# Performance work log

Measured on AMD Instinct MI355X. Metric: run time of the kernel, lower is better.

Reference implementation:

```python
import jax, jax.numpy as jnp
import numpy as np

N = 100000      # nodes
E = 1600000     # edges
IN = 64         # in_feats
H = 64          # h_feats
L = 4           # num_conv_layers
FC = 2          # num_fc_layers
G = 512         # num graphs in batch
EPS = 1e-5      # BatchNorm eps


def _bn(x, g, b):
    # training-mode BatchNorm1d: batch stats (biased variance), affine
    m = x.mean(axis=0)
    v = x.var(axis=0)
    return (x - m) * jax.lax.rsqrt(v + EPS) * g + b


def setup_inputs() -> dict:
    key = jax.random.key(0)
    ks = jax.random.split(key, 12)
    x = jax.random.normal(ks[0], (N, IN), jnp.float32)
    edge_index = jax.random.randint(ks[1], (2, E), 0, N)
    batch = jnp.sort(jax.random.randint(ks[2], (N,), 0, G))
    s_in = 1.0 / np.sqrt(IN)
    s_h = 1.0 / np.sqrt(H)
    return {
        "x": x,
        "edge_index": edge_index,
        "batch": batch,
        "bn_feat_g": jnp.ones((IN,), jnp.float32),
        "bn_feat_b": jnp.zeros((IN,), jnp.float32),
        "lin_feat_W": jax.random.normal(ks[3], (IN, H), jnp.float32) * s_in,
        "lin_feat_b": jnp.zeros((H,), jnp.float32),
        "bn_conv_g": jnp.ones((L, H), jnp.float32),
        "bn_conv_b": jnp.zeros((L, H), jnp.float32),
        "conv_W": jax.random.normal(ks[4], (L, H, H), jnp.float32) * s_h,
        "conv_b": jnp.zeros((L, H), jnp.float32),
        "bn_fc_g": jnp.ones((FC, H), jnp.float32),
        "bn_fc_b": jnp.zeros((FC, H), jnp.float32),
        "fc_W": jax.random.normal(ks[5], (FC, H, H), jnp.float32) * s_h,
        "fc_b": jnp.zeros((FC, H), jnp.float32),
        "bn_hid_g": jnp.ones((H,), jnp.float32),
        "bn_hid_b": jnp.zeros((H,), jnp.float32),
    }


def reference(x, edge_index, batch, bn_feat_g, bn_feat_b, lin_feat_W, lin_feat_b,
              bn_conv_g, bn_conv_b, conv_W, conv_b, bn_fc_g, bn_fc_b, fc_W, fc_b,
              bn_hid_g, bn_hid_b):
    # --- GCN symmetric normalization with self-loops (computed once) ---
    loop = jnp.arange(N)
    src = jnp.concatenate([edge_index[0], loop])   # source j
    dst = jnp.concatenate([edge_index[1], loop])   # target i
    deg = jax.ops.segment_sum(jnp.ones((E + N,), x.dtype), dst, num_segments=N)
    dinv = jnp.where(deg > 0, 1.0, 0.0) / jnp.sqrt(jnp.where(deg > 0, deg, 1.0))
    norm = dinv[src] * dinv[dst]                   # [E+N]

    # --- stem ---
    h = _bn(x, bn_feat_g, bn_feat_b)
    h = jax.nn.relu(h @ lin_feat_W + lin_feat_b)

    # --- stacked GCNConv + BN + ReLU + residual ---
    for i in range(L):
        h_ = _bn(h, bn_conv_g[i], bn_conv_b[i])
        m = h_ @ conv_W[i]                                    # [N,H]
        agg = jax.ops.segment_sum(norm[:, None] * m[src], dst, num_segments=N)
        h = h + jax.nn.relu(agg + conv_b[i])                  # residual=True

    # --- global add pool over graphs ---
    h = jax.ops.segment_sum(h, batch, num_segments=G)         # [G,H]

    # --- fc head ---
    for i in range(FC):
        h_ = _bn(h, bn_fc_g[i], bn_fc_b[i])
        h = jax.nn.relu(h_ @ fc_W[i] + fc_b[i])

    return _bn(h, bn_hid_g, bn_hid_b)
```

## Files before the change

kernel.cpp:

```cpp
#include <hip/hip_runtime.h>
#include <hip/hip_bf16.h>

#define NN 100000
#define EE 1600000
#define GG 512
#define NB ((NN + 255) / 256)

__global__ void deg_kernel(const int* __restrict__ ei, int* __restrict__ cnt, int E_) {
    int e = blockIdx.x * 256 + threadIdx.x;
    if (e < E_) atomicAdd(&cnt[ei[E_ + e]], 1);
}

__global__ void dinv_kernel(const int* __restrict__ cnt, float* __restrict__ dinv, int n) {
    int i = blockIdx.x * 256 + threadIdx.x;
    if (i < n) dinv[i] = rsqrtf((float)cnt[i] + 1.0f);
}

__global__ void blocksum(const int* __restrict__ cnt, int* __restrict__ bsum) {
    __shared__ int sh[256];
    int i = blockIdx.x * 256 + threadIdx.x;
    sh[threadIdx.x] = (i < NN) ? cnt[i] : 0;
    __syncthreads();
    for (int o = 128; o > 0; o >>= 1) {
        if (threadIdx.x < o) sh[threadIdx.x] += sh[threadIdx.x + o];
        __syncthreads();
    }
    if (threadIdx.x == 0) bsum[blockIdx.x] = sh[0];
}

__global__ void scan_bsum(int* __restrict__ bsum, int nb) {
    __shared__ int sh[512];
    int t = threadIdx.x;
    int v = (t < nb) ? bsum[t] : 0;
    int orig = v;
    sh[t] = v;
    __syncthreads();
    for (int o = 1; o < 512; o <<= 1) {
        int add = (t >= o) ? sh[t - o] : 0;
        __syncthreads();
        sh[t] += add;
        __syncthreads();
    }
    if (t < nb) bsum[t] = sh[t] - orig;
}

__global__ void scan_final(const int* __restrict__ cnt, const int* __restrict__ boff,
                           int* __restrict__ row_ptr, int* __restrict__ cursor) {
    __shared__ int sh[256];
    int i = blockIdx.x * 256 + threadIdx.x;
    int v = (i < NN) ? cnt[i] : 0;
    int orig = v;
    sh[threadIdx.x] = v;
    __syncthreads();
    for (int o = 1; o < 256; o <<= 1) {
        int add = (threadIdx.x >= o) ? sh[threadIdx.x - o] : 0;
        __syncthreads();
        sh[threadIdx.x] += add;
        __syncthreads();
    }
    if (i < NN) {
        int ex = boff[blockIdx.x] + sh[threadIdx.x] - orig;
        row_ptr[i] = ex;
        cursor[i] = ex;
    }
    if (i == 0) row_ptr[NN] = EE;
}

__global__ void fill_csr(const int* __restrict__ ei, const float* __restrict__ dinv,
                         int* __restrict__ cursor, int* __restrict__ csr_src,
                         float* __restrict__ csr_norm, int E_) {
    int e = blockIdx.x * 256 + threadIdx.x;
    if (e < E_) {
        int s = ei[e], d = ei[E_ + e];
        int pos = atomicAdd(&cursor[d], 1);
        csr_src[pos] = s;
        csr_norm[pos] = dinv[s] * dinv[d];
    }
}

__global__ void colstats(const float* __restrict__ A, int nrows, float* __restrict__ stats) {
    __shared__ float ssum[4][64];
    __shared__ float ssq[4][64];
    int tid = threadIdx.x;
    int col = tid & 63, rg = tid >> 6;
    float s = 0.f, q = 0.f;
    for (int r = blockIdx.x * 4 + rg; r < nrows; r += gridDim.x * 4) {
        float v = A[r * 64 + col];
        s += v;
        q = fmaf(v, v, q);
    }
    ssum[rg][col] = s; ssq[rg][col] = q;
    __syncthreads();
    if (tid < 64) {
        float ts = ssum[0][tid] + ssum[1][tid] + ssum[2][tid] + ssum[3][tid];
        float tq = ssq[0][tid] + ssq[1][tid] + ssq[2][tid] + ssq[3][tid];
        atomicAdd(&stats[tid], ts);
        atomicAdd(&stats[64 + tid], tq);
    }
}

__global__ void prep(const float* __restrict__ stats, float count,
                     const float* __restrict__ g, const float* __restrict__ b,
                     const float* __restrict__ W, const float* __restrict__ basebias,
                     float* __restrict__ Wp, float* __restrict__ bp) {
    int j = threadIdx.x;
    float acc = basebias ? basebias[j] : 0.f;
    for (int k = 0; k < 64; k++) {
        float mu  = stats[k] / count;
        float var = fmaxf(stats[64 + k] / count - mu * mu, 0.f);
        float rstd = rsqrtf(var + 1e-5f);
        float a = rstd * g[k];
        float w = W[k * 64 + j];
        Wp[k * 64 + j] = a * w;
        acc = fmaf(b[k] - mu * a, w, acc);
    }
    bp[j] = acc;
}

__global__ __launch_bounds__(256) void gemm64(const float* __restrict__ A,
                                              const float* __restrict__ Wp,
                                              const float* __restrict__ bp,
                                              float* __restrict__ C, int nrows, int dorelu,
                                              float* __restrict__ stats) {
    __shared__ float Ws[64 * 64];
    __shared__ float As[64 * 64];
    __shared__ float ssh[256];
    __shared__ float qsh[256];
    int tid = threadIdx.x;
    int row0 = blockIdx.x * 64;
    for (int i = tid; i < 4096; i += 256) {
        Ws[i] = Wp[i];
        int r = row0 + (i >> 6);
        As[i] = (r < nrows) ? A[row0 * 64 + i] : 0.f;
    }
    __syncthreads();
    int col = tid & 63;
    int rg = tid >> 6;
    float bcol = bp[col];
    float s = 0.f, q = 0.f;
    for (int rr = rg; rr < 64; rr += 4) {
        int r = row0 + rr;
        if (r >= nrows) break;
        float acc = bcol;
#pragma unroll
        for (int k = 0; k < 64; k++) acc = fmaf(As[rr * 64 + k], Ws[k * 64 + col], acc);
        float v = dorelu ? fmaxf(acc, 0.f) : acc;
        C[r * 64 + col] = v;
        s += v;
        q = fmaf(v, v, q);
    }
    if (stats) {
        ssh[tid] = s; qsh[tid] = q;
        __syncthreads();
        if (tid < 64) {
            float ts = ssh[tid] + ssh[64 + tid] + ssh[128 + tid] + ssh[192 + tid];
            float tq = qsh[tid] + qsh[64 + tid] + qsh[128 + tid] + qsh[192 + tid];
            atomicAdd(&stats[tid], ts);
            atomicAdd(&stats[64 + tid], tq);
        }
    }
}

__global__ __launch_bounds__(256) void gather(const int* __restrict__ row_ptr,
                                              const int* __restrict__ csr_src,
                                              const float* __restrict__ csr_norm,
                                              const float* __restrict__ dinv,
                                              const float* __restrict__ m,
                                              float* __restrict__ h,
                                              const float* __restrict__ cb,
                                              float* __restrict__ stats,
                                              float* __restrict__ pooled,
                                              const int* __restrict__ batch,
                                              int writeH) {
    int tid = threadIdx.x;
    int ng = tid >> 4;
    int cl = tid & 15;
    const float4* cb4 = (const float4*)cb;
    float4 cbv = cb4[cl];
    float sx = 0.f, sy = 0.f, sz = 0.f, sw = 0.f;
    float qx = 0.f, qy = 0.f, qz = 0.f, qw = 0.f;
    for (int i = blockIdx.x * 16 + ng; i < NN; i += gridDim.x * 16) {
        float di = dinv[i];
        float4 mi = ((const float4*)(m + i * 64))[cl];
        float d2 = di * di;
        float ax = d2 * mi.x, ay = d2 * mi.y, az = d2 * mi.z, aw = d2 * mi.w;
        int e0 = row_ptr[i], e1 = row_ptr[i + 1];
        for (int e = e0; e < e1; e++) {
            int s = csr_src[e];
            float w = csr_norm[e];
            float4 ms = ((const float4*)(m + s * 64))[cl];
            ax = fmaf(w, ms.x, ax);
            ay = fmaf(w, ms.y, ay);
            az = fmaf(w, ms.z, az);
            aw = fmaf(w, ms.w, aw);
        }
        float4 hb = ((const float4*)(h + i * 64))[cl];
        float nx = hb.x + fmaxf(ax + cbv.x, 0.f);
        float ny = hb.y + fmaxf(ay + cbv.y, 0.f);
        float nz = hb.z + fmaxf(az + cbv.z, 0.f);
        float nw = hb.w + fmaxf(aw + cbv.w, 0.f);
        if (writeH) {
            float4 o; o.x = nx; o.y = ny; o.z = nz; o.w = nw;
            ((float4*)(h + i * 64))[cl] = o;
        }
        if (stats) {
            sx += nx; sy += ny; sz += nz; sw += nw;
            qx = fmaf(nx, nx, qx); qy = fmaf(ny, ny, qy);
            qz = fmaf(nz, nz, qz); qw = fmaf(nw, nw, qw);
        }
        if (pooled) {
            int g = batch[i];
            float* p = pooled + g * 64 + cl * 4;
            atomicAdd(p + 0, nx);
            atomicAdd(p + 1, ny);
            atomicAdd(p + 2, nz);
            atomicAdd(p + 3, nw);
        }
    }
    if (stats) {
        __shared__ float rs[256 * 4];
        __shared__ float rq[256 * 4];
        rs[tid * 4 + 0] = sx; rs[tid * 4 + 1] = sy; rs[tid * 4 + 2] = sz; rs[tid * 4 + 3] = sw;
        rq[tid * 4 + 0] = qx; rq[tid * 4 + 1] = qy; rq[tid * 4 + 2] = qz; rq[tid * 4 + 3] = qw;
        __syncthreads();
        if (tid < 64) {
            int cl2 = tid >> 2, k = tid & 3;
            float a = 0.f, b = 0.f;
            for (int g = 0; g < 16; g++) {
                a += rs[(g * 16 + cl2) * 4 + k];
                b += rq[(g * 16 + cl2) * 4 + k];
            }
            atomicAdd(&stats[tid], a);
            atomicAdd(&stats[64 + tid], b);
        }
    }
}

__global__ void bn_apply(const float* __restrict__ A, const float* __restrict__ stats, float count,
                         const float* __restrict__ g, const float* __restrict__ b,
                         float* __restrict__ out, int total) {
    int idx = blockIdx.x * 256 + threadIdx.x;
    if (idx < total) {
        int j = idx & 63;
        float mu  = stats[j] / count;
        float var = fmaxf(stats[64 + j] / count - mu * mu, 0.f);
        float rstd = rsqrtf(var + 1e-5f);
        out[idx] = (A[idx] - mu) * rstd * g[j] + b[j];
    }
}

extern "C" void kernel_launch(void* const* d_in, const int* in_sizes, int n_in,
                              void* d_out, int out_size, void* d_ws, size_t ws_size,
                              hipStream_t stream) {
    const float* x     = (const float*)d_in[0];
    const int*   ei    = (const int*)d_in[1];
    const int*   batch = (const int*)d_in[2];
    const float* bnfg  = (const float*)d_in[3];
    const float* bnfb  = (const float*)d_in[4];
    const float* linW  = (const float*)d_in[5];
    const float* linb  = (const float*)d_in[6];
    const float* bncg  = (const float*)d_in[7];
    const float* bncb  = (const float*)d_in[8];
    const float* convW = (const float*)d_in[9];
    const float* convb = (const float*)d_in[10];
    const float* bnfcg = (const float*)d_in[11];
    const float* bnfcb = (const float*)d_in[12];
    const float* fcW   = (const float*)d_in[13];
    const float* fcb   = (const float*)d_in[14];
    const float* bnhg  = (const float*)d_in[15];
    const float* bnhb  = (const float*)d_in[16];

    const int N64 = NN * 64;
    float* ws = (float*)d_ws;
    size_t o = 0;
    int*   cnt      = (int*)(ws + o);   o += 100352;
    float* dinv     = ws + o;           o += 100352;
    int*   row_ptr  = (int*)(ws + o);   o += 100352;
    int*   cursor   = (int*)(ws + o);   o += 100352;
    int*   bsum     = (int*)(ws + o);   o += 512;
    int*   csr_src  = (int*)(ws + o);   o += EE;
    float* csr_norm = ws + o;           o += EE;
    float* h        = ws + o;           o += N64;
    float* m        = ws + o;           o += N64;
    float* statsA   = ws + o;           o += 128;
    float* statsB   = ws + o;           o += 128;
    float* Wp       = ws + o;           o += 4096;
    float* bp       = ws + o;           o += 64;
    float* pa       = ws + o;           o += GG * 64;
    float* pb       = ws + o;           o += GG * 64;

    hipMemsetAsync(cnt, 0, NN * sizeof(int), stream);
    deg_kernel<<<(EE + 255) / 256, 256, 0, stream>>>(ei, cnt, EE);
    dinv_kernel<<<NB, 256, 0, stream>>>(cnt, dinv, NN);
    blocksum<<<NB, 256, 0, stream>>>(cnt, bsum);
    scan_bsum<<<1, 512, 0, stream>>>(bsum, NB);
    scan_final<<<NB, 256, 0, stream>>>(cnt, bsum, row_ptr, cursor);
    fill_csr<<<(EE + 255) / 256, 256, 0, stream>>>(ei, dinv, cursor, csr_src, csr_norm, EE);

    hipMemsetAsync(statsA, 0, 512, stream);
    colstats<<<256, 256, 0, stream>>>(x, NN, statsA);
    prep<<<1, 64, 0, stream>>>(statsA, (float)NN, bnfg, bnfb, linW, linb, Wp, bp);
    hipMemsetAsync(statsB, 0, 512, stream);
    gemm64<<<(NN + 63) / 64, 256, 0, stream>>>(x, Wp, bp, h, NN, 1, statsB);

    hipMemsetAsync(pa, 0, GG * 64 * sizeof(float), stream);
    float* cur = statsB; float* nxt = statsA;
    for (int l = 0; l < 4; l++) {
        prep<<<1, 64, 0, stream>>>(cur, (float)NN, bncg + 64 * l, bncb + 64 * l,
                                   convW + 4096 * l, nullptr, Wp, bp);
        gemm64<<<(NN + 63) / 64, 256, 0, stream>>>(h, Wp, bp, m, NN, 0, nullptr);
        if (l < 3) {
            hipMemsetAsync(nxt, 0, 512, stream);
            gather<<<1024, 256, 0, stream>>>(row_ptr, csr_src, csr_norm, dinv, m, h,
                                             convb + 64 * l, nxt, nullptr, batch, 1);
        } else {
            gather<<<1024, 256, 0, stream>>>(row_ptr, csr_src, csr_norm, dinv, m, h,
                                             convb + 64 * l, nullptr, pa, batch, 0);
        }
        float* t = cur; cur = nxt; nxt = t;
    }

    float* pin = pa; float* pout = pb;
    for (int i = 0; i < 2; i++) {
        hipMemsetAsync(statsA, 0, 512, stream);
        colstats<<<8, 256, 0, stream>>>(pin, GG, statsA);
        prep<<<1, 64, 0, stream>>>(statsA, (float)GG, bnfcg + 64 * i, bnfcb + 64 * i,
                                   fcW + 4096 * i, fcb + 64 * i, Wp, bp);
        gemm64<<<(GG + 63) / 64, 256, 0, stream>>>(pin, Wp, bp, pout, GG, 1, nullptr);
        float* t = pin; pin = pout; pout = t;
    }

    hipMemsetAsync(statsA, 0, 512, stream);
    colstats<<<8, 256, 0, stream>>>(pin, GG, statsA);
    bn_apply<<<(GG * 64 + 255) / 256, 256, 0, stream>>>(pin, statsA, (float)GG, bnhg, bnhb,
                                                        (float*)d_out, GG * 64);
}
```

Baseline: 1.290 ms.

## Interleave CSR src/norm, unroll gather edge loop, one node per thread group

```diff
diff --git a/kernel.cpp b/kernel.cpp
--- a/kernel.cpp
+++ b/kernel.cpp
@@ -67,14 +67,15 @@
 }
 
 __global__ void fill_csr(const int* __restrict__ ei, const float* __restrict__ dinv,
-                         int* __restrict__ cursor, int* __restrict__ csr_src,
-                         float* __restrict__ csr_norm, int E_) {
+                         int* __restrict__ cursor, float2* __restrict__ ent, int E_) {
     int e = blockIdx.x * 256 + threadIdx.x;
     if (e < E_) {
         int s = ei[e], d = ei[E_ + e];
         int pos = atomicAdd(&cursor[d], 1);
-        csr_src[pos] = s;
-        csr_norm[pos] = dinv[s] * dinv[d];
+        float2 v;
+        v.x = __int_as_float(s);
+        v.y = dinv[s] * dinv[d];
+        ent[pos] = v;
     }
 }
 
@@ -162,8 +163,7 @@
 }
 
 __global__ __launch_bounds__(256) void gather(const int* __restrict__ row_ptr,
-                                              const int* __restrict__ csr_src,
-                                              const float* __restrict__ csr_norm,
+                                              const float2* __restrict__ ent,
                                               const float* __restrict__ dinv,
                                               const float* __restrict__ m,
                                               float* __restrict__ h,
@@ -175,53 +175,78 @@
     int tid = threadIdx.x;
     int ng = tid >> 4;
     int cl = tid & 15;
-    const float4* cb4 = (const float4*)cb;
-    float4 cbv = cb4[cl];
-    float sx = 0.f, sy = 0.f, sz = 0.f, sw = 0.f;
-    float qx = 0.f, qy = 0.f, qz = 0.f, qw = 0.f;
-    for (int i = blockIdx.x * 16 + ng; i < NN; i += gridDim.x * 16) {
-        float di = dinv[i];
-        float4 mi = ((const float4*)(m + i * 64))[cl];
-        float d2 = di * di;
-        float ax = d2 * mi.x, ay = d2 * mi.y, az = d2 * mi.z, aw = d2 * mi.w;
-        int e0 = row_ptr[i], e1 = row_ptr[i + 1];
-        for (int e = e0; e < e1; e++) {
-            int s = csr_src[e];
-            float w = csr_norm[e];
-            float4 ms = ((const float4*)(m + s * 64))[cl];
-            ax = fmaf(w, ms.x, ax);
-            ay = fmaf(w, ms.y, ay);
-            az = fmaf(w, ms.z, az);
-            aw = fmaf(w, ms.w, aw);
-        }
-        float4 hb = ((const float4*)(h + i * 64))[cl];
-        float nx = hb.x + fmaxf(ax + cbv.x, 0.f);
-        float ny = hb.y + fmaxf(ay + cbv.y, 0.f);
-        float nz = hb.z + fmaxf(az + cbv.z, 0.f);
-        float nw = hb.w + fmaxf(aw + cbv.w, 0.f);
-        if (writeH) {
-            float4 o; o.x = nx; o.y = ny; o.z = nz; o.w = nw;
-            ((float4*)(h + i * 64))[cl] = o;
-        }
-        if (stats) {
-            sx += nx; sy += ny; sz += nz; sw += nw;
-            qx = fmaf(nx, nx, qx); qy = fmaf(ny, ny, qy);
-            qz = fmaf(nz, nz, qz); qw = fmaf(nw, nw, qw);
-        }
-        if (pooled) {
-            int g = batch[i];
-            float* p = pooled + g * 64 + cl * 4;
-            atomicAdd(p + 0, nx);
-            atomicAdd(p + 1, ny);
-            atomicAdd(p + 2, nz);
-            atomicAdd(p + 3, nw);
-        }
+    const float4* m4 = (const float4*)m;
+    float4 cbv = ((const float4*)cb)[cl];
+    int i = blockIdx.x * 16 + ng;
+
+    float di = dinv[i];
+    float4 mi = m4[i * 16 + cl];
+    float d2 = di * di;
+    float ax = d2 * mi.x, ay = d2 * mi.y, az = d2 * mi.z, aw = d2 * mi.w;
+    int e = row_ptr[i], e1 = row_ptr[i + 1];
+
+    for (; e + 8 <= e1; e += 8) {
+        float2 c0 = ent[e + 0], c1 = ent[e + 1], c2 = ent[e + 2], c3 = ent[e + 3];
+        float2 c4 = ent[e + 4], c5 = ent[e + 5], c6 = ent[e + 6], c7 = ent[e + 7];
+        float4 r0 = m4[__float_as_int(c0.x) * 16 + cl];
+        float4 r1 = m4[__float_as_int(c1.x) * 16 + cl];
+        float4 r2 = m4[__float_as_int(c2.x) * 16 + cl];
+        float4 r3 = m4[__float_as_int(c3.x) * 16 + cl];
+        float4 r4 = m4[__float_as_int(c4.x) * 16 + cl];
+        float4 r5 = m4[__float_as_int(c5.x) * 16 + cl];
+        float4 r6 = m4[__float_as_int(c6.x) * 16 + cl];
+        float4 r7 = m4[__float_as_int(c7.x) * 16 + cl];
+        ax = fmaf(c0.y, r0.x, ax); ay = fmaf(c0.y, r0.y, ay); az = fmaf(c0.y, r0.z, az); aw = fmaf(c0.y, r0.w, aw);
+        ax = fmaf(c1.y, r1.x, ax); ay = fmaf(c1.y, r1.y, ay); az = fmaf(c1.y, r1.z, az); aw = fmaf(c1.y, r1.w, aw);
+        ax = fmaf(c2.y, r2.x, ax); ay = fmaf(c2.y, r2.y, ay); az = fmaf(c2.y, r2.z, az); aw = fmaf(c2.y, r2.w, aw);
+        ax = fmaf(c3.y, r3.x, ax); ay = fmaf(c3.y, r3.y, ay); az = fmaf(c3.y, r3.z, az); aw = fmaf(c3.y, r3.w, aw);
+        ax = fmaf(c4.y, r4.x, ax); ay = fmaf(c4.y, r4.y, ay); az = fmaf(c4.y, r4.z, az); aw = fmaf(c4.y, r4.w, aw);
+        ax = fmaf(c5.y, r5.x, ax); ay = fmaf(c5.y, r5.y, ay); az = fmaf(c5.y, r5.z, az); aw = fmaf(c5.y, r5.w, aw);
+        ax = fmaf(c6.y, r6.x, ax); ay = fmaf(c6.y, r6.y, ay); az = fmaf(c6.y, r6.z, az); aw = fmaf(c6.y, r6.w, aw);
+        ax = fmaf(c7.y, r7.x, ax); ay = fmaf(c7.y, r7.y, ay); az = fmaf(c7.y, r7.z, az); aw = fmaf(c7.y, r7.w, aw);
+    }
+    if (e + 4 <= e1) {
+        float2 c0 = ent[e + 0], c1 = ent[e + 1], c2 = ent[e + 2], c3 = ent[e + 3];
+        float4 r0 = m4[__float_as_int(c0.x) * 16 + cl];
+        float4 r1 = m4[__float_as_int(c1.x) * 16 + cl];
+        float4 r2 = m4[__float_as_int(c2.x) * 16 + cl];
+        float4 r3 = m4[__float_as_int(c3.x) * 16 + cl];
+        ax = fmaf(c0.y, r0.x, ax); ay = fmaf(c0.y, r0.y, ay); az = fmaf(c0.y, r0.z, az); aw = fmaf(c0.y, r0.w, aw);
+        ax = fmaf(c1.y, r1.x, ax); ay = fmaf(c1.y, r1.y, ay); az = fmaf(c1.y, r1.z, az); aw = fmaf(c1.y, r1.w, aw);
+        ax = fmaf(c2.y, r2.x, ax); ay = fmaf(c2.y, r2.y, ay); az = fmaf(c2.y, r2.z, az); aw = fmaf(c2.y, r2.w, aw);
+        ax = fmaf(c3.y, r3.x, ax); ay = fmaf(c3.y, r3.y, ay); az = fmaf(c3.y, r3.z, az); aw = fmaf(c3.y, r3.w, aw);
+        e += 4;
+    }
+    for (; e < e1; e++) {
+        float2 c = ent[e];
+        float4 r = m4[__float_as_int(c.x) * 16 + cl];
+        ax = fmaf(c.y, r.x, ax); ay = fmaf(c.y, r.y, ay);
+        az = fmaf(c.y, r.z, az); aw = fmaf(c.y, r.w, aw);
+    }
+
+    float4 hb = ((const float4*)h)[i * 16 + cl];
+    float nx = hb.x + fmaxf(ax + cbv.x, 0.f);
+    float ny = hb.y + fmaxf(ay + cbv.y, 0.f);
+    float nz = hb.z + fmaxf(az + cbv.z, 0.f);
+    float nw = hb.w + fmaxf(aw + cbv.w, 0.f);
+    if (writeH) {
+        float4 o; o.x = nx; o.y = ny; o.z = nz; o.w = nw;
+        ((float4*)h)[i * 16 + cl] = o;
+    }
+    if (pooled) {
+        int g = batch[i];
+        float* p = pooled + g * 64 + cl * 4;
+        atomicAdd(p + 0, nx);
+        atomicAdd(p + 1, ny);
+        atomicAdd(p + 2, nz);
+        atomicAdd(p + 3, nw);
     }
     if (stats) {
         __shared__ float rs[256 * 4];
         __shared__ float rq[256 * 4];
-        rs[tid * 4 + 0] = sx; rs[tid * 4 + 1] = sy; rs[tid * 4 + 2] = sz; rs[tid * 4 + 3] = sw;
-        rq[tid * 4 + 0] = qx; rq[tid * 4 + 1] = qy; rq[tid * 4 + 2] = qz; rq[tid * 4 + 3] = qw;
+        rs[tid * 4 + 0] = nx; rs[tid * 4 + 1] = ny; rs[tid * 4 + 2] = nz; rs[tid * 4 + 3] = nw;
+        rq[tid * 4 + 0] = nx * nx; rq[tid * 4 + 1] = ny * ny;
+        rq[tid * 4 + 2] = nz * nz; rq[tid * 4 + 3] = nw * nw;
         __syncthreads();
         if (tid < 64) {
             int cl2 = tid >> 2, k = tid & 3;
@@ -273,21 +298,20 @@
     const int N64 = NN * 64;
     float* ws = (float*)d_ws;
     size_t o = 0;
-    int*   cnt      = (int*)(ws + o);   o += 100352;
-    float* dinv     = ws + o;           o += 100352;
-    int*   row_ptr  = (int*)(ws + o);   o += 100352;
-    int*   cursor   = (int*)(ws + o);   o += 100352;
-    int*   bsum     = (int*)(ws + o);   o += 512;
-    int*   csr_src  = (int*)(ws + o);   o += EE;
-    float* csr_norm = ws + o;           o += EE;
-    float* h        = ws + o;           o += N64;
-    float* m        = ws + o;           o += N64;
-    float* statsA   = ws + o;           o += 128;
-    float* statsB   = ws + o;           o += 128;
-    float* Wp       = ws + o;           o += 4096;
-    float* bp       = ws + o;           o += 64;
-    float* pa       = ws + o;           o += GG * 64;
-    float* pb       = ws + o;           o += GG * 64;
+    int*    cnt     = (int*)(ws + o);    o += 100352;
+    float*  dinv    = ws + o;            o += 100352;
+    int*    row_ptr = (int*)(ws + o);    o += 100352;
+    int*    cursor  = (int*)(ws + o);    o += 100352;
+    int*    bsum    = (int*)(ws + o);    o += 512;
+    float2* ent     = (float2*)(ws + o); o += 2 * (size_t)EE;
+    float*  h       = ws + o;            o += N64;
+    float*  m       = ws + o;            o += N64;
+    float*  statsA  = ws + o;            o += 128;
+    float*  statsB  = ws + o;            o += 128;
+    float*  Wp      = ws + o;            o += 4096;
+    float*  bp      = ws + o;            o += 64;
+    float*  pa      = ws + o;            o += GG * 64;
+    float*  pb      = ws + o;            o += GG * 64;
 
     hipMemsetAsync(cnt, 0, NN * sizeof(int), stream);
     deg_kernel<<<(EE + 255) / 256, 256, 0, stream>>>(ei, cnt, EE);
@@ -295,7 +319,7 @@
     blocksum<<<NB, 256, 0, stream>>>(cnt, bsum);
     scan_bsum<<<1, 512, 0, stream>>>(bsum, NB);
     scan_final<<<NB, 256, 0, stream>>>(cnt, bsum, row_ptr, cursor);
-    fill_csr<<<(EE + 255) / 256, 256, 0, stream>>>(ei, dinv, cursor, csr_src, csr_norm, EE);
+    fill_csr<<<(EE + 255) / 256, 256, 0, stream>>>(ei, dinv, cursor, ent, EE);
 
     hipMemsetAsync(statsA, 0, 512, stream);
     colstats<<<256, 256, 0, stream>>>(x, NN, statsA);
@@ -311,11 +335,11 @@
         gemm64<<<(NN + 63) / 64, 256, 0, stream>>>(h, Wp, bp, m, NN, 0, nullptr);
         if (l < 3) {
             hipMemsetAsync(nxt, 0, 512, stream);
-            gather<<<1024, 256, 0, stream>>>(row_ptr, csr_src, csr_norm, dinv, m, h,
-                                             convb + 64 * l, nxt, nullptr, batch, 1);
+            gather<<<NN / 16, 256, 0, stream>>>(row_ptr, ent, dinv, m, h,
+                                                convb + 64 * l, nxt, nullptr, batch, 1);
         } else {
-            gather<<<1024, 256, 0, stream>>>(row_ptr, csr_src, csr_norm, dinv, m, h,
-                                             convb + 64 * l, nullptr, pa, batch, 0);
+            gather<<<NN / 16, 256, 0, stream>>>(row_ptr, ent, dinv, m, h,
+                                                convb + 64 * l, nullptr, pa, batch, 0);
         }
         float* t = cur; cur = nxt; nxt = t;
     }
```

Result: slower. 1.437 ms (+11.4%).
